# Optimization experiments

Hardware: AMD Instinct MI355X
Metric: run time of the kernel (lower is better)

## Reference

```python
import jax, jax.numpy as jnp
import numpy as np

B, T, D, H = 4, 2048, 1024, 16
HD = D // H  # head_size = 64


def setup_inputs() -> dict:
    key = jax.random.key(0)
    ks = jax.random.split(key, 6)
    s = 0.02
    x = jax.random.normal(ks[0], (B, T, D), dtype=jnp.float32)
    # per-head unfused projections, stacked over heads: [H, D, HD]
    Wq = jax.random.normal(ks[1], (H, D, HD), dtype=jnp.float32) * s
    Wk = jax.random.normal(ks[2], (H, D, HD), dtype=jnp.float32) * s
    Wv = jax.random.normal(ks[3], (H, D, HD), dtype=jnp.float32) * s
    # output projection, torch Linear layout [out, in]
    Wo = jax.random.normal(ks[4], (D, D), dtype=jnp.float32) * s
    bo = jax.random.normal(ks[5], (D,), dtype=jnp.float32) * s
    return {"x": x, "Wq": Wq, "Wk": Wk, "Wv": Wv, "Wo": Wo, "bo": bo}


def reference(x, Wq, Wk, Wv, Wo, bo):
    b, t, d = x.shape
    hd = Wq.shape[-1]
    q = jnp.einsum('btd,hdk->bhtk', x, Wq)
    k = jnp.einsum('btd,hdk->bhtk', x, Wk)
    v = jnp.einsum('btd,hdk->bhtk', x, Wv)
    scores = jnp.einsum('bhtk,bhsk->bhts', q, k) / jnp.sqrt(jnp.float32(hd))
    mask = jnp.tril(jnp.ones((t, t), dtype=bool))  # causal
    scores = jnp.where(mask, scores, jnp.float32(-jnp.inf))
    p = jax.nn.softmax(scores, axis=-1)
    o = jnp.einsum('bhts,bhsk->bhtk', p, v)
    o = o.transpose(0, 2, 1, 3).reshape(b, t, d)  # concat heads
    return o @ Wo.T + bo
```

## Files before the change

kernel.cpp:

```cpp
#include <hip/hip_runtime.h>
#include <hip/hip_bf16.h>
#include <stdint.h>

#define B_   4
#define T_   2048
#define D_   1024
#define H_   16
#define HD_  64
#define MROWS (B_*T_)
#define NQKV  3072
#define NST  (T_/64)

typedef __attribute__((ext_vector_type(8))) short  short8;
typedef __attribute__((ext_vector_type(4))) short  bf16x4;
typedef __attribute__((ext_vector_type(4))) float  floatx4;

#define QSCALE 0.1803368801111244f

__device__ inline void async_copy16(const __hip_bfloat16* g, __hip_bfloat16* l) {
  __builtin_amdgcn_global_load_lds(
      (const __attribute__((address_space(1))) void*)g,
      (__attribute__((address_space(3))) void*)l, 16, 0, 0);
}

__device__ inline floatx4 mfma16(bf16x4 a, bf16x4 b, floatx4 c) {
#if __has_builtin(__builtin_amdgcn_mfma_f32_16x16x16bf16_1k)
  return __builtin_amdgcn_mfma_f32_16x16x16bf16_1k(a, b, c, 0, 0, 0);
#elif __has_builtin(__builtin_amdgcn_mfma_f32_16x16x16_bf16)
  return __builtin_amdgcn_mfma_f32_16x16x16_bf16(a, b, c, 0, 0, 0);
#else
  short8 a8 = (short8){a[0], a[1], a[2], a[3], 0, 0, 0, 0};
  short8 b8 = (short8){b[0], b[1], b[2], b[3], 0, 0, 0, 0};
  return __builtin_amdgcn_mfma_f32_16x16x32_bf16(a8, b8, c, 0, 0, 0);
#endif
}


__global__ void convert_bf16(const float* __restrict__ in, __hip_bfloat16* __restrict__ out, int n) {
  int i = (blockIdx.x * blockDim.x + threadIdx.x) * 4;
  if (i < n) {
    float4 v = *(const float4*)(in + i);
    out[i + 0] = __float2bfloat16(v.x);
    out[i + 1] = __float2bfloat16(v.y);
    out[i + 2] = __float2bfloat16(v.z);
    out[i + 3] = __float2bfloat16(v.w);
  }
}

__global__ void transpose_w(const float* __restrict__ Wq, const float* __restrict__ Wk,
                            const float* __restrict__ Wv, __hip_bfloat16* __restrict__ wqkv) {
  __shared__ __hip_bfloat16 tile[64][65];
  const int t = threadIdx.x;
  const int d0 = blockIdx.x * 64;
  const int wh = blockIdx.y;
  const int which = wh >> 4, h = wh & 15;
  const float* W = (which == 0) ? Wq : ((which == 1) ? Wk : Wv);
  const float* base = W + (size_t)h * D_ * HD_;
#pragma unroll
  for (int i = 0; i < 16; i++) {
    int e = i * 256 + t;
    int dr = e >> 6, hd = e & 63;
    tile[dr][hd] = __float2bfloat16(base[(size_t)(d0 + dr) * HD_ + hd]);
  }
  __syncthreads();
#pragma unroll
  for (int i = 0; i < 16; i++) {
    int e = i * 256 + t;
    int hd = e >> 6, dr = e & 63;
    wqkv[(size_t)(which * 1024 + h * 64 + hd) * D_ + d0 + dr] = tile[dr][hd];
  }
}

__global__ void repack_kv(const __hip_bfloat16* __restrict__ qkv,
                          __hip_bfloat16* __restrict__ kpack, __hip_bfloat16* __restrict__ vpack) {
  __shared__ __hip_bfloat16 Ks[64][72];
  __shared__ __hip_bfloat16 Vs[64][72];
  const int tid = threadIdx.x;
  const int st = blockIdx.x, bh = blockIdx.y;
  const int b = bh >> 4, h = bh & 15;
#pragma unroll
  for (int p = 0; p < 2; p++) {
    int c = p * 256 + tid;
    int row = c >> 3, col8 = c & 7;
    const __hip_bfloat16* src = qkv + (size_t)(b * T_ + st * 64 + row) * NQKV + h * HD_ + col8 * 8;
    *(uint4*)&Ks[row][col8 * 8] = *(const uint4*)(src + 1024);
    *(uint4*)&Vs[row][col8 * 8] = *(const uint4*)(src + 2048);
  }
  __syncthreads();
  const size_t base = ((size_t)bh * NST + st) * 8 * 512;
#pragma unroll
  for (int p = 0; p < 2; p++) {
    int pair = p * 256 + tid;
    int c = pair >> 6, l = pair & 63;
    int lq = l & 15, q = l >> 4;
    int ni = c >> 1, half = c & 1;
    short8 v = *(const short8*)&Ks[ni * 16 + lq][half * 32 + q * 8];
    *(short8*)(kpack + base + (size_t)c * 512 + l * 8) = v;
  }
#pragma unroll
  for (int p = 0; p < 2; p++) {
    int pair = p * 256 + tid;
    int c = pair >> 6, l = pair & 63;
    int lq = l & 15, q = l >> 4;
    int m = c >> 2, nt = c & 3;
    __hip_bfloat16 tmp[8];
#pragma unroll
    for (int half = 0; half < 2; half++)
#pragma unroll
      for (int j = 0; j < 4; j++)
        tmp[half * 4 + j] = Vs[(2 * m + half) * 16 + q * 4 + j][nt * 16 + lq];
    *(short8*)(vpack + base + (size_t)c * 512 + l * 8) = *(short8*)tmp;
  }
}

template <int EPI>
__launch_bounds__(256, 2)
__global__ void gemm_bt(const __hip_bfloat16* __restrict__ A, const __hip_bfloat16* __restrict__ Bt,
                        __hip_bfloat16* __restrict__ Cb, float* __restrict__ Cf,
                        const float* __restrict__ bias, int M, int N, int K, float qscale) {
  __shared__ __hip_bfloat16 As[128 * 32];
  __shared__ __hip_bfloat16 Bs[128 * 32];
  const int tid = threadIdx.x;
  const int w = tid >> 6, lane = tid & 63;
  const int lq = lane & 15, quad = lane >> 4;
  const int wr = w >> 1, wc = w & 1;
  const int m0 = blockIdx.x * 128, n0 = blockIdx.y * 128;

  floatx4 acc[4][4];
#pragma unroll
  for (int i = 0; i < 4; i++)
#pragma unroll
    for (int j = 0; j < 4; j++) acc[i][j] = (floatx4){0.f, 0.f, 0.f, 0.f};

  for (int k0 = 0; k0 < K; k0 += 32) {
    __syncthreads();
#pragma unroll
    for (int ph = 0; ph < 2; ++ph) {
      int c = ph * 256 + tid;
      int row = c >> 2, col8 = c & 3;
      async_copy16(A + (size_t)(m0 + row) * K + k0 + col8 * 8, As + c * 8);
      async_copy16(Bt + (size_t)(n0 + row) * K + k0 + col8 * 8, Bs + c * 8);
    }
    __syncthreads();
    short8 af[4], bf[4];
#pragma unroll
    for (int mi = 0; mi < 4; mi++)
      af[mi] = *(const short8*)(As + (wr * 64 + mi * 16 + lq) * 32 + quad * 8);
#pragma unroll
    for (int ni = 0; ni < 4; ni++)
      bf[ni] = *(const short8*)(Bs + (wc * 64 + ni * 16 + lq) * 32 + quad * 8);
#pragma unroll
    for (int mi = 0; mi < 4; mi++)
#pragma unroll
      for (int ni = 0; ni < 4; ni++)
        acc[mi][ni] = __builtin_amdgcn_mfma_f32_16x16x32_bf16(af[mi], bf[ni], acc[mi][ni], 0, 0, 0);
  }

#pragma unroll
  for (int mi = 0; mi < 4; mi++) {
#pragma unroll
    for (int ni = 0; ni < 4; ni++) {
      int col = n0 + wc * 64 + ni * 16 + lq;
      if (EPI == 0) {
        float s = (col < 1024) ? qscale : 1.0f;
#pragma unroll
        for (int r = 0; r < 4; r++) {
          int row = m0 + wr * 64 + mi * 16 + quad * 4 + r;
          Cb[(size_t)row * N + col] = __float2bfloat16(acc[mi][ni][r] * s);
        }
      } else {
        float bv = bias[col];
#pragma unroll
        for (int r = 0; r < 4; r++) {
          int row = m0 + wr * 64 + mi * 16 + quad * 4 + r;
          Cf[(size_t)row * N + col] = acc[mi][ni][r] + bv;
        }
      }
    }
  }
}

__launch_bounds__(256, 2)
__global__ void attn(const __hip_bfloat16* __restrict__ qkv,
                     const __hip_bfloat16* __restrict__ kpack,
                     const __hip_bfloat16* __restrict__ vpack,
                     __hip_bfloat16* __restrict__ obuf) {
  const int tid = threadIdx.x;
  const int w = tid >> 6, lane = tid & 63;
  const int lq = lane & 15, quad = lane >> 4;

  const int bh = (int)blockIdx.x;
  const int a  = (int)blockIdx.y;
  const int b = bh >> 4, h = bh & 15;

  const __hip_bfloat16* kb0 = kpack + ((size_t)bh * NST) * 4096 + lane * 8;
  const __hip_bfloat16* vb0 = vpack + ((size_t)bh * NST) * 4096 + lane * 8;

#pragma unroll 1
  for (int seg = 0; seg < 2; ++seg) {
    const int tbase = seg ? (NST - 2 - 2 * a) : (2 * a);
    const int qt = tbase + (w >> 1);
    const int rbase = (w & 1) * 32;

    short8 qf[2][2];
#pragma unroll
    for (int bi = 0; bi < 2; bi++) {
      const __hip_bfloat16* qp =
          qkv + ((size_t)(b * T_ + qt * 64 + rbase + bi * 16 + lq)) * NQKV + h * HD_;
      qf[bi][0] = *(const short8*)(qp + quad * 8);
      qf[bi][1] = *(const short8*)(qp + 32 + quad * 8);
    }

    floatx4 Oacc[2][4];
#pragma unroll
    for (int bi = 0; bi < 2; bi++)
#pragma unroll
      for (int i = 0; i < 4; i++) Oacc[bi][i] = (floatx4){0.f, 0.f, 0.f, 0.f};
    float lrow[2] = {0.f, 0.f};

    const __hip_bfloat16* kb = kb0;
    const __hip_bfloat16* vb = vb0;
    const int nIter = qt + 1;
    for (int it = 0; it < nIter; ++it) {
      short8 kf[4], kg[4];
#pragma unroll
      for (int ni = 0; ni < 4; ni++) {
        kf[ni] = *(const short8*)(kb + (size_t)(ni * 2 + 0) * 512);
        kg[ni] = *(const short8*)(kb + (size_t)(ni * 2 + 1) * 512);
      }
      short8 vfr[8];
#pragma unroll
      for (int c = 0; c < 8; c++) vfr[c] = *(const short8*)(vb + (size_t)c * 512);

      floatx4 Sc[2][4];
#pragma unroll
      for (int bi = 0; bi < 2; bi++)
#pragma unroll
        for (int ni = 0; ni < 4; ni++) {
          floatx4 c0 = (floatx4){0.f, 0.f, 0.f, 0.f};
          c0 = __builtin_amdgcn_mfma_f32_16x16x32_bf16(kf[ni], qf[bi][0], c0, 0, 0, 0);
          c0 = __builtin_amdgcn_mfma_f32_16x16x32_bf16(kg[ni], qf[bi][1], c0, 0, 0, 0);
          Sc[bi][ni] = c0;
        }

      if (it == nIter - 1) {
#pragma unroll
        for (int bi = 0; bi < 2; bi++) {
          int lrow_idx = rbase + bi * 16 + lq;
#pragma unroll
          for (int ni = 0; ni < 4; ni++)
#pragma unroll
            for (int r = 0; r < 4; r++) {
              int s_loc = ni * 16 + quad * 4 + r;
              if (s_loc > lrow_idx) Sc[bi][ni][r] = -__builtin_inff();
            }
        }
      }

      bf16x4 pf[2][4];
#pragma unroll
      for (int bi = 0; bi < 2; bi++)
#pragma unroll
        for (int c = 0; c < 4; c++) {
          __hip_bfloat16 pb[4];
#pragma unroll
          for (int r = 0; r < 4; r++) {
            float p = __builtin_amdgcn_exp2f(Sc[bi][c][r]);
            lrow[bi] += p;
            pb[r] = __float2bfloat16(p);
          }
          pf[bi][c] = *(bf16x4*)pb;
        }

#pragma unroll
      for (int m = 0; m < 2; m++)
#pragma unroll
        for (int nt = 0; nt < 4; nt++) {
          short8 v8 = vfr[m * 4 + nt];
          bf16x4 vlo = (bf16x4){v8[0], v8[1], v8[2], v8[3]};
          bf16x4 vhi = (bf16x4){v8[4], v8[5], v8[6], v8[7]};
#pragma unroll
          for (int bi = 0; bi < 2; bi++) {
            Oacc[bi][nt] = mfma16(pf[bi][2 * m + 0], vlo, Oacc[bi][nt]);
            Oacc[bi][nt] = mfma16(pf[bi][2 * m + 1], vhi, Oacc[bi][nt]);
          }
        }

      kb += 4096;
      vb += 4096;
    }

#pragma unroll
    for (int bi = 0; bi < 2; bi++) {
      float ps = lrow[bi];
      ps += __shfl_xor(ps, 16);
      ps += __shfl_xor(ps, 32);
      float inv = 1.0f / ps;
#pragma unroll
      for (int r = 0; r < 4; r++) {
        float invr = __shfl(inv, quad * 4 + r);
        int t = qt * 64 + rbase + bi * 16 + quad * 4 + r;
#pragma unroll
        for (int nt = 0; nt < 4; nt++)
          obuf[(size_t)(b * T_ + t) * D_ + h * HD_ + nt * 16 + lq] =
              __float2bfloat16(Oacc[bi][nt][r] * invr);
      }
    }
  }
}


extern "C" void kernel_launch(void* const* d_in, const int* in_sizes, int n_in,
                              void* d_out, int out_size, void* d_ws, size_t ws_size,
                              hipStream_t stream) {
  const float* x  = (const float*)d_in[0];
  const float* Wq = (const float*)d_in[1];
  const float* Wk = (const float*)d_in[2];
  const float* Wv = (const float*)d_in[3];
  const float* Wo = (const float*)d_in[4];
  const float* bo = (const float*)d_in[5];
  float* out = (float*)d_out;

  char* ws = (char*)d_ws;
  __hip_bfloat16* xb    = (__hip_bfloat16*)(ws);
  __hip_bfloat16* obuf  = (__hip_bfloat16*)(ws);
  __hip_bfloat16* wqkv  = (__hip_bfloat16*)(ws + ((size_t)16 << 20));
  __hip_bfloat16* wob   = (__hip_bfloat16*)(ws + ((size_t)22 << 20));
  __hip_bfloat16* qkv   = (__hip_bfloat16*)(ws + ((size_t)24 << 20));
  __hip_bfloat16* kpack = (__hip_bfloat16*)(ws + ((size_t)72 << 20));
  __hip_bfloat16* vpack = (__hip_bfloat16*)(ws + ((size_t)88 << 20));

  convert_bf16<<<(MROWS * D_) / 1024, 256, 0, stream>>>(x, xb, MROWS * D_);
  convert_bf16<<<(D_ * D_) / 1024, 256, 0, stream>>>(Wo, wob, D_ * D_);
  transpose_w<<<dim3(16, 48), 256, 0, stream>>>(Wq, Wk, Wv, wqkv);

  gemm_bt<0><<<dim3(MROWS / 128, NQKV / 128), 256, 0, stream>>>(
      xb, wqkv, qkv, nullptr, nullptr, MROWS, NQKV, D_, QSCALE);

  repack_kv<<<dim3(NST, B_ * H_), 256, 0, stream>>>(qkv, kpack, vpack);

  attn<<<dim3(B_ * H_, 8), 256, 0, stream>>>(qkv, kpack, vpack, obuf);

  gemm_bt<1><<<dim3(MROWS / 128, D_ / 128), 256, 0, stream>>>(
      obuf, wob, nullptr, out, bo, MROWS, D_, D_, 1.0f);
}
```

Measured before the change: 248.4 us.

## Replace QKV projection GEMM with 256x256 pipelined eight-wave kernel

Adds a new gemm8 kernel for the QKV projection. It uses 256x256 tiles with 512 threads, double-buffered LDS filled by async global-to-LDS copies with an XOR swizzle, and phases MFMA work interleaved with the next tile's loads under priority hints. It also remaps workgroups for better cache locality. This aims to raise MFMA utilization and hide memory latency compared with the 128x128 gemm_bt. The cost is large LDS use (128KB per block) and complex hand-placed waitcnt and barrier scheduling that could hurt occupancy or correctness if misordered.

```diff
diff --git a/kernel.cpp b/kernel.cpp
--- a/kernel.cpp
+++ b/kernel.cpp
@@ -110,6 +110,134 @@
       for (int j = 0; j < 4; j++)
         tmp[half * 4 + j] = Vs[(2 * m + half) * 16 + q * 4 + j][nt * 16 + lq];
     *(short8*)(vpack + base + (size_t)c * 512 + l * 8) = *(short8*)tmp;
+  }
+}
+
+
+__device__ inline void stage_half(const __hip_bfloat16* __restrict__ gsrc, int ldk,
+                                  short* ldst, int tid) {
+#pragma unroll
+  for (int l = 0; l < 2; ++l) {
+    int c = l * 512 + tid;
+    int row = c >> 3;
+    int sce = ((((c & 7) << 4) ^ ((row & 7) << 4)) >> 1);
+    async_copy16(gsrc + (size_t)row * ldk + sce, (__hip_bfloat16*)(ldst + c * 8));
+  }
+}
+
+__device__ inline short8 fragld(const short* base, int row, int kk, int quad) {
+  int c2 = ((kk << 6) | (quad << 4)) ^ ((row & 7) << 4);
+  return *(const short8*)(base + row * 64 + (c2 >> 1));
+}
+
+#define LOAD_A(MQ) \
+  _Pragma("unroll") for (int mi = 0; mi < 4; ++mi) \
+  _Pragma("unroll") for (int kk = 0; kk < 2; ++kk) \
+    a[mi][kk] = fragld(Ab, wr * 128 + (MQ) * 64 + mi * 16 + lq, kk, quad);
+
+#define LOAD_B(DST, NQ) \
+  _Pragma("unroll") for (int ni = 0; ni < 2; ++ni) \
+  _Pragma("unroll") for (int kk = 0; kk < 2; ++kk) \
+    DST[ni][kk] = fragld(Bb, wc * 64 + (NQ) * 32 + ni * 16 + lq, kk, quad);
+
+#define QUAD_MFMA(M0, N0, BREG) \
+  _Pragma("unroll") for (int kk = 0; kk < 2; ++kk) \
+  _Pragma("unroll") for (int mi = 0; mi < 4; ++mi) \
+  _Pragma("unroll") for (int ni = 0; ni < 2; ++ni) \
+    acc[(M0) + mi][(N0) + ni] = __builtin_amdgcn_mfma_f32_16x16x32_bf16( \
+        a[mi][kk], BREG[ni][kk], acc[(M0) + mi][(N0) + ni], 0, 0, 0);
+
+#define PH_SYNC_BEGIN() \
+  __builtin_amdgcn_s_barrier(); \
+  asm volatile("s_waitcnt lgkmcnt(0)" ::: "memory"); \
+  __builtin_amdgcn_s_setprio(1);
+
+#define PH_SYNC_END() \
+  __builtin_amdgcn_s_setprio(0); \
+  __builtin_amdgcn_s_barrier();
+
+__launch_bounds__(512, 2)
+__global__ void gemm8(const __hip_bfloat16* __restrict__ A, const __hip_bfloat16* __restrict__ Bt,
+                      __hip_bfloat16* __restrict__ Cb, int M, int N, int K, float qscale) {
+  __shared__ short As[2][16384];
+  __shared__ short Bs[2][16384];
+  const int tid = threadIdx.x;
+  const int lane = tid & 63, wid = tid >> 6;
+  const int lq = lane & 15, quad = lane >> 4;
+  const int wr = wid >> 2, wc = wid & 3;
+
+  const int nbx = gridDim.x, nwg = gridDim.x * gridDim.y;
+  int lin = blockIdx.y * nbx + blockIdx.x;
+  int s = (nwg & 7) ? lin : ((lin & 7) * (nwg >> 3) + (lin >> 3));
+  const int m0 = (s % nbx) * 256, n0 = (s / nbx) * 256;
+
+  const int NT = K >> 6;
+
+  stage_half(Bt + (size_t)n0 * K, K, &Bs[0][0], tid);
+  stage_half(A + (size_t)m0 * K, K, &As[0][0], tid);
+  stage_half(A + (size_t)(m0 + 128) * K, K, &As[0][8192], tid);
+  stage_half(Bt + (size_t)(n0 + 128) * K, K, &Bs[0][8192], tid);
+  stage_half(Bt + (size_t)n0 * K + 64, K, &Bs[1][0], tid);
+  stage_half(A + (size_t)m0 * K + 64, K, &As[1][0], tid);
+
+  floatx4 acc[8][4];
+#pragma unroll
+  for (int i = 0; i < 8; i++)
+#pragma unroll
+    for (int j = 0; j < 4; j++) acc[i][j] = (floatx4){0.f, 0.f, 0.f, 0.f};
+
+  asm volatile("s_waitcnt vmcnt(4)" ::: "memory");
+  __builtin_amdgcn_s_barrier();
+
+  for (int t = 0; t < NT; ++t) {
+    const int buf = t & 1, nbuf = buf ^ 1;
+    const short* Ab = As[buf];
+    const short* Bb = Bs[buf];
+    const int kc1 = (t + 1) << 6, kc2 = (t + 2) << 6;
+    short8 a[4][2], b0[2][2], b1[2][2];
+
+    LOAD_A(0);
+    LOAD_B(b0, 0);
+    if (t + 1 < NT) stage_half(A + (size_t)(m0 + 128) * K + kc1, K, &As[nbuf][8192], tid);
+    PH_SYNC_BEGIN();
+    QUAD_MFMA(0, 0, b0);
+    PH_SYNC_END();
+
+    LOAD_B(b1, 1);
+    if (t + 1 < NT) stage_half(Bt + (size_t)(n0 + 128) * K + kc1, K, &Bs[nbuf][8192], tid);
+    PH_SYNC_BEGIN();
+    QUAD_MFMA(0, 2, b1);
+    PH_SYNC_END();
+
+    LOAD_A(1);
+    if (t + 2 < NT) stage_half(Bt + (size_t)n0 * K + kc2, K, &Bs[buf][0], tid);
+    PH_SYNC_BEGIN();
+    QUAD_MFMA(4, 2, b1);
+    PH_SYNC_END();
+
+    if (t + 2 < NT) stage_half(A + (size_t)m0 * K + kc2, K, &As[buf][0], tid);
+    __builtin_amdgcn_s_barrier();
+    asm volatile("s_waitcnt lgkmcnt(0)" ::: "memory");
+    __builtin_amdgcn_s_setprio(1);
+    QUAD_MFMA(4, 0, b0);
+    __builtin_amdgcn_s_setprio(0);
+    if (t + 2 < NT) { asm volatile("s_waitcnt vmcnt(4)" ::: "memory"); }
+    else            { asm volatile("s_waitcnt vmcnt(0)" ::: "memory"); }
+    __builtin_amdgcn_s_barrier();
+  }
+
+#pragma unroll
+  for (int mi = 0; mi < 8; ++mi) {
+#pragma unroll
+    for (int ni = 0; ni < 4; ++ni) {
+      int col = n0 + wc * 64 + ni * 16 + lq;
+      float sc = (col < 1024) ? qscale : 1.0f;
+#pragma unroll
+      for (int r = 0; r < 4; ++r) {
+        int row = m0 + wr * 128 + mi * 16 + quad * 4 + r;
+        Cb[(size_t)row * N + col] = __float2bfloat16(acc[mi][ni][r] * sc);
+      }
+    }
   }
 }
 
@@ -334,8 +462,8 @@
   convert_bf16<<<(D_ * D_) / 1024, 256, 0, stream>>>(Wo, wob, D_ * D_);
   transpose_w<<<dim3(16, 48), 256, 0, stream>>>(Wq, Wk, Wv, wqkv);
 
-  gemm_bt<0><<<dim3(MROWS / 128, NQKV / 128), 256, 0, stream>>>(
-      xb, wqkv, qkv, nullptr, nullptr, MROWS, NQKV, D_, QSCALE);
+  gemm8<<<dim3(MROWS / 256, NQKV / 256), 512, 0, stream>>>(
+      xb, wqkv, qkv, MROWS, NQKV, D_, QSCALE);
 
   repack_kv<<<dim3(NST, B_ * H_), 256, 0, stream>>>(qkv, kpack, vpack);
 
```

Result: slower. 257.6 us (+3.7%).

## Stage K/V tiles in LDS with async double buffering and fuse prep kernels

Applied to the files above, without the earlier changes.

The attention kernel now loads each K/V tile once per block into shared memory with global_load_lds, double-buffered, so the next tile is prefetched while the current one is computed. Before, each wave read K/V fragments straight from global memory. The four waves working on different query tiles now share a single load, and the loop runs to the pair's top tile with a __syncthreads each iteration. MFMA sections are wrapped in s_setprio. The three preprocessing launches (two converts and the weight transpose) are merged into one kernel to cut launch overhead. The per-iteration barriers and uneven causal work inside a block may add stalls.

```diff
diff --git a/kernel.cpp b/kernel.cpp
--- a/kernel.cpp
+++ b/kernel.cpp
@@ -35,39 +35,48 @@
 #endif
 }
 
-
-__global__ void convert_bf16(const float* __restrict__ in, __hip_bfloat16* __restrict__ out, int n) {
-  int i = (blockIdx.x * blockDim.x + threadIdx.x) * 4;
-  if (i < n) {
-    float4 v = *(const float4*)(in + i);
-    out[i + 0] = __float2bfloat16(v.x);
-    out[i + 1] = __float2bfloat16(v.y);
-    out[i + 2] = __float2bfloat16(v.z);
-    out[i + 3] = __float2bfloat16(v.w);
-  }
-}
-
-__global__ void transpose_w(const float* __restrict__ Wq, const float* __restrict__ Wk,
-                            const float* __restrict__ Wv, __hip_bfloat16* __restrict__ wqkv) {
+__global__ void prep(const float* __restrict__ x, const float* __restrict__ Wo,
+                     const float* __restrict__ Wq, const float* __restrict__ Wk,
+                     const float* __restrict__ Wv,
+                     __hip_bfloat16* __restrict__ xb, __hip_bfloat16* __restrict__ wob,
+                     __hip_bfloat16* __restrict__ wqkv) {
   __shared__ __hip_bfloat16 tile[64][65];
+  const int bid = (int)blockIdx.x;
   const int t = threadIdx.x;
-  const int d0 = blockIdx.x * 64;
-  const int wh = blockIdx.y;
-  const int which = wh >> 4, h = wh & 15;
-  const float* W = (which == 0) ? Wq : ((which == 1) ? Wk : Wv);
-  const float* base = W + (size_t)h * D_ * HD_;
-#pragma unroll
-  for (int i = 0; i < 16; i++) {
-    int e = i * 256 + t;
-    int dr = e >> 6, hd = e & 63;
-    tile[dr][hd] = __float2bfloat16(base[(size_t)(d0 + dr) * HD_ + hd]);
-  }
-  __syncthreads();
-#pragma unroll
-  for (int i = 0; i < 16; i++) {
-    int e = i * 256 + t;
-    int hd = e >> 6, dr = e & 63;
-    wqkv[(size_t)(which * 1024 + h * 64 + hd) * D_ + d0 + dr] = tile[dr][hd];
+  if (bid < 8192) {
+    int i = (bid * 256 + t) * 4;
+    float4 v = *(const float4*)(x + i);
+    xb[i + 0] = __float2bfloat16(v.x);
+    xb[i + 1] = __float2bfloat16(v.y);
+    xb[i + 2] = __float2bfloat16(v.z);
+    xb[i + 3] = __float2bfloat16(v.w);
+  } else if (bid < 9216) {
+    int i = ((bid - 8192) * 256 + t) * 4;
+    float4 v = *(const float4*)(Wo + i);
+    wob[i + 0] = __float2bfloat16(v.x);
+    wob[i + 1] = __float2bfloat16(v.y);
+    wob[i + 2] = __float2bfloat16(v.z);
+    wob[i + 3] = __float2bfloat16(v.w);
+  } else {
+    int idx = bid - 9216;
+    const int d0 = (idx & 15) * 64;
+    const int wh = idx >> 4;
+    const int which = wh >> 4, h = wh & 15;
+    const float* W = (which == 0) ? Wq : ((which == 1) ? Wk : Wv);
+    const float* base = W + (size_t)h * D_ * HD_;
+#pragma unroll
+    for (int i = 0; i < 16; i++) {
+      int e = i * 256 + t;
+      int dr = e >> 6, hd = e & 63;
+      tile[dr][hd] = __float2bfloat16(base[(size_t)(d0 + dr) * HD_ + hd]);
+    }
+    __syncthreads();
+#pragma unroll
+    for (int i = 0; i < 16; i++) {
+      int e = i * 256 + t;
+      int hd = e >> 6, dr = e & 63;
+      wqkv[(size_t)(which * 1024 + h * 64 + hd) * D_ + d0 + dr] = tile[dr][hd];
+    }
   }
 }
 
@@ -185,6 +194,7 @@
                      const __hip_bfloat16* __restrict__ kpack,
                      const __hip_bfloat16* __restrict__ vpack,
                      __hip_bfloat16* __restrict__ obuf) {
+  __shared__ __hip_bfloat16 KVs[2][8192];
   const int tid = threadIdx.x;
   const int w = tid >> 6, lane = tid & 63;
   const int lq = lane & 15, quad = lane >> 4;
@@ -193,8 +203,8 @@
   const int a  = (int)blockIdx.y;
   const int b = bh >> 4, h = bh & 15;
 
-  const __hip_bfloat16* kb0 = kpack + ((size_t)bh * NST) * 4096 + lane * 8;
-  const __hip_bfloat16* vb0 = vpack + ((size_t)bh * NST) * 4096 + lane * 8;
+  const __hip_bfloat16* kbase = kpack + ((size_t)bh * NST) * 4096;
+  const __hip_bfloat16* vbase = vpack + ((size_t)bh * NST) * 4096;
 
 #pragma unroll 1
   for (int seg = 0; seg < 2; ++seg) {
@@ -218,76 +228,101 @@
       for (int i = 0; i < 4; i++) Oacc[bi][i] = (floatx4){0.f, 0.f, 0.f, 0.f};
     float lrow[2] = {0.f, 0.f};
 
-    const __hip_bfloat16* kb = kb0;
-    const __hip_bfloat16* vb = vb0;
-    const int nIter = qt + 1;
-    for (int it = 0; it < nIter; ++it) {
-      short8 kf[4], kg[4];
-#pragma unroll
-      for (int ni = 0; ni < 4; ni++) {
-        kf[ni] = *(const short8*)(kb + (size_t)(ni * 2 + 0) * 512);
-        kg[ni] = *(const short8*)(kb + (size_t)(ni * 2 + 1) * 512);
+    const int itTop = tbase + 1;
+
+#pragma unroll
+    for (int j = 0; j < 2; ++j) {
+      int c = j * 256 + tid;
+      async_copy16(kbase + (size_t)c * 8, &KVs[0][0] + c * 8);
+      async_copy16(vbase + (size_t)c * 8, &KVs[0][4096] + c * 8);
+    }
+    __syncthreads();
+
+#pragma unroll 1
+    for (int it = 0; it <= itTop; ++it) {
+      const int cur = it & 1;
+      if (it < itTop) {
+        const __hip_bfloat16* kn = kbase + (size_t)(it + 1) * 4096;
+        const __hip_bfloat16* vn = vbase + (size_t)(it + 1) * 4096;
+#pragma unroll
+        for (int j = 0; j < 2; ++j) {
+          int c = j * 256 + tid;
+          async_copy16(kn + (size_t)c * 8, &KVs[cur ^ 1][0] + c * 8);
+          async_copy16(vn + (size_t)c * 8, &KVs[cur ^ 1][4096] + c * 8);
+        }
       }
-      short8 vfr[8];
-#pragma unroll
-      for (int c = 0; c < 8; c++) vfr[c] = *(const short8*)(vb + (size_t)c * 512);
-
-      floatx4 Sc[2][4];
-#pragma unroll
-      for (int bi = 0; bi < 2; bi++)
+      if (it <= qt) {
+        const __hip_bfloat16* Kb = &KVs[cur][0] + lane * 8;
+        const __hip_bfloat16* Vb = &KVs[cur][4096] + lane * 8;
+        short8 kf[4], kg[4];
 #pragma unroll
         for (int ni = 0; ni < 4; ni++) {
-          floatx4 c0 = (floatx4){0.f, 0.f, 0.f, 0.f};
-          c0 = __builtin_amdgcn_mfma_f32_16x16x32_bf16(kf[ni], qf[bi][0], c0, 0, 0, 0);
-          c0 = __builtin_amdgcn_mfma_f32_16x16x32_bf16(kg[ni], qf[bi][1], c0, 0, 0, 0);
-          Sc[bi][ni] = c0;
-        }
-
-      if (it == nIter - 1) {
-#pragma unroll
-        for (int bi = 0; bi < 2; bi++) {
-          int lrow_idx = rbase + bi * 16 + lq;
-#pragma unroll
-          for (int ni = 0; ni < 4; ni++)
+          kf[ni] = *(const short8*)(Kb + (size_t)(ni * 2 + 0) * 512);
+          kg[ni] = *(const short8*)(Kb + (size_t)(ni * 2 + 1) * 512);
+        }
+        short8 vfr[8];
+#pragma unroll
+        for (int c = 0; c < 8; c++) vfr[c] = *(const short8*)(Vb + (size_t)c * 512);
+
+        floatx4 Sc[2][4];
+        __builtin_amdgcn_s_setprio(1);
+#pragma unroll
+        for (int bi = 0; bi < 2; bi++)
+#pragma unroll
+          for (int ni = 0; ni < 4; ni++) {
+            floatx4 c0 = (floatx4){0.f, 0.f, 0.f, 0.f};
+            c0 = __builtin_amdgcn_mfma_f32_16x16x32_bf16(kf[ni], qf[bi][0], c0, 0, 0, 0);
+            c0 = __builtin_amdgcn_mfma_f32_16x16x32_bf16(kg[ni], qf[bi][1], c0, 0, 0, 0);
+            Sc[bi][ni] = c0;
+          }
+        __builtin_amdgcn_s_setprio(0);
+
+        if (it == qt) {
+#pragma unroll
+          for (int bi = 0; bi < 2; bi++) {
+            int lrow_idx = rbase + bi * 16 + lq;
+#pragma unroll
+            for (int ni = 0; ni < 4; ni++)
+#pragma unroll
+              for (int r = 0; r < 4; r++) {
+                int s_loc = ni * 16 + quad * 4 + r;
+                if (s_loc > lrow_idx) Sc[bi][ni][r] = -__builtin_inff();
+              }
+          }
+        }
+
+        bf16x4 pf[2][4];
+#pragma unroll
+        for (int bi = 0; bi < 2; bi++)
+#pragma unroll
+          for (int c = 0; c < 4; c++) {
+            __hip_bfloat16 pb[4];
 #pragma unroll
             for (int r = 0; r < 4; r++) {
-              int s_loc = ni * 16 + quad * 4 + r;
-              if (s_loc > lrow_idx) Sc[bi][ni][r] = -__builtin_inff();
+              float p = __builtin_amdgcn_exp2f(Sc[bi][c][r]);
+              lrow[bi] += p;
+              pb[r] = __float2bfloat16(p);
             }
-        }
+            pf[bi][c] = *(bf16x4*)pb;
+          }
+
+        __builtin_amdgcn_s_setprio(1);
+#pragma unroll
+        for (int m = 0; m < 2; m++)
+#pragma unroll
+          for (int nt = 0; nt < 4; nt++) {
+            short8 v8 = vfr[m * 4 + nt];
+            bf16x4 vlo = (bf16x4){v8[0], v8[1], v8[2], v8[3]};
+            bf16x4 vhi = (bf16x4){v8[4], v8[5], v8[6], v8[7]};
+#pragma unroll
+            for (int bi = 0; bi < 2; bi++) {
+              Oacc[bi][nt] = mfma16(pf[bi][2 * m + 0], vlo, Oacc[bi][nt]);
+              Oacc[bi][nt] = mfma16(pf[bi][2 * m + 1], vhi, Oacc[bi][nt]);
+            }
+          }
+        __builtin_amdgcn_s_setprio(0);
       }
-
-      bf16x4 pf[2][4];
-#pragma unroll
-      for (int bi = 0; bi < 2; bi++)
-#pragma unroll
-        for (int c = 0; c < 4; c++) {
-          __hip_bfloat16 pb[4];
-#pragma unroll
-          for (int r = 0; r < 4; r++) {
-            float p = __builtin_amdgcn_exp2f(Sc[bi][c][r]);
-            lrow[bi] += p;
-            pb[r] = __float2bfloat16(p);
-          }
-          pf[bi][c] = *(bf16x4*)pb;
-        }
-
-#pragma unroll
-      for (int m = 0; m < 2; m++)
-#pragma unroll
-        for (int nt = 0; nt < 4; nt++) {
-          short8 v8 = vfr[m * 4 + nt];
-          bf16x4 vlo = (bf16x4){v8[0], v8[1], v8[2], v8[3]};
-          bf16x4 vhi = (bf16x4){v8[4], v8[5], v8[6], v8[7]};
-#pragma unroll
-          for (int bi = 0; bi < 2; bi++) {
-            Oacc[bi][nt] = mfma16(pf[bi][2 * m + 0], vlo, Oacc[bi][nt]);
-            Oacc[bi][nt] = mfma16(pf[bi][2 * m + 1], vhi, Oacc[bi][nt]);
-          }
-        }
-
-      kb += 4096;
-      vb += 4096;
+      __syncthreads();
     }
 
 #pragma unroll
@@ -330,9 +365,7 @@
   __hip_bfloat16* kpack = (__hip_bfloat16*)(ws + ((size_t)72 << 20));
   __hip_bfloat16* vpack = (__hip_bfloat16*)(ws + ((size_t)88 << 20));
 
-  convert_bf16<<<(MROWS * D_) / 1024, 256, 0, stream>>>(x, xb, MROWS * D_);
-  convert_bf16<<<(D_ * D_) / 1024, 256, 0, stream>>>(Wo, wob, D_ * D_);
-  transpose_w<<<dim3(16, 48), 256, 0, stream>>>(Wq, Wk, Wv, wqkv);
+  prep<<<9984, 256, 0, stream>>>(x, Wo, Wq, Wk, Wv, xb, wob, wqkv);
 
   gemm_bt<0><<<dim3(MROWS / 128, NQKV / 128), 256, 0, stream>>>(
       xb, wqkv, qkv, nullptr, nullptr, MROWS, NQKV, D_, QSCALE);
```

Measured after the change: 248.7 us. Within noise of the previous version (+0.1%).
